# Kernel tuning notes

Hardware: AMD Instinct MI355X
Metric: run time of the kernel (lower is better)

Reference implementation:

```python
import jax, jax.numpy as jnp
import numpy as np

NPOINT, RADIUS, NSAMPLE = 512, 0.2, 32
MLP = [64, 64, 128]
IN_CH = 67
EPS = 1e-5


def farthest_point_sample(xyz, npoint):
    # xyz: [B, N, 3] -> idx [B, npoint]. Deterministic start at index 0.
    B, N, _ = xyz.shape

    def step(carry, _):
        dist, far = carry  # dist [B,N], far [B]
        centroid = jnp.take_along_axis(xyz, far[:, None, None], axis=1)  # [B,1,3]
        d = jnp.sum((xyz - centroid) ** 2, axis=-1)  # [B,N]
        dist = jnp.minimum(dist, d)
        return (dist, jnp.argmax(dist, axis=-1).astype(jnp.int32)), far

    init = (jnp.full((B, N), 1e10, dtype=xyz.dtype), jnp.zeros((B,), jnp.int32))
    _, idxs = jax.lax.scan(step, init, None, length=npoint)
    return idxs.T  # [B, npoint]


def query_ball_point(radius, nsample, xyz, new_xyz):
    # xyz [B,N,3], new_xyz [B,S,3] -> idx [B,S,nsample]
    B, N, _ = xyz.shape
    sqr = jnp.sum((new_xyz[:, :, None, :] - xyz[:, None, :, :]) ** 2, axis=-1)  # [B,S,N]
    gidx = jnp.where(sqr > radius * radius, N, jnp.arange(N, dtype=jnp.int32))
    gidx = jnp.sort(gidx, axis=-1)[:, :, :nsample]
    first = gidx[:, :, :1]
    return jnp.where(gidx == N, first, gidx).astype(jnp.int32)


def gather_points(pts, idx):
    # pts [B,N,C], idx [B,...] -> [B,...,C]
    return jax.vmap(lambda p, i: p[i])(pts, idx)


def sample_and_group(npoint, radius, nsample, xyz, points):
    fps_idx = farthest_point_sample(xyz, npoint)          # [B,S]
    new_xyz = gather_points(xyz, fps_idx)                 # [B,S,3]
    idx = query_ball_point(radius, nsample, xyz, new_xyz)  # [B,S,K]
    grouped_xyz = gather_points(xyz, idx)                 # [B,S,K,3]
    grouped_xyz_norm = grouped_xyz - new_xyz[:, :, None, :]
    grouped_pts = gather_points(points, idx)              # [B,S,K,D]
    new_points = jnp.concatenate([grouped_xyz_norm, grouped_pts], axis=-1)  # [B,S,K,3+D]
    return new_xyz, new_points


def mlp_bn_relu(x, w, b, gamma, beta):
    # x [B,C,K,S]; 1x1 conv + training-mode BatchNorm2d + ReLU
    y = jnp.einsum('oc,bcks->boks', w, x) + b[None, :, None, None]
    mean = jnp.mean(y, axis=(0, 2, 3), keepdims=True)
    var = jnp.var(y, axis=(0, 2, 3), keepdims=True)
    y = (y - mean) * jax.lax.rsqrt(var + EPS)
    y = y * gamma[None, :, None, None] + beta[None, :, None, None]
    return jax.nn.relu(y)


def setup_inputs() -> dict:
    key = jax.random.key(0)
    ks = jax.random.split(key, 8)
    B, N, D = 16, 2048, 64
    inp = {
        'xyz': jax.random.normal(ks[0], (B, 3, N), jnp.float32),
        'points': jax.random.normal(ks[1], (B, D, N), jnp.float32),
    }
    last = IN_CH
    for i, out in enumerate(MLP):
        kw = jax.random.fold_in(ks[2], i)
        inp[f'w{i}'] = jax.random.normal(kw, (out, last), jnp.float32) * 0.05
        inp[f'b{i}'] = jnp.zeros((out,), jnp.float32)
        inp[f'g{i}'] = jnp.ones((out,), jnp.float32)
        inp[f'bt{i}'] = jnp.zeros((out,), jnp.float32)
        last = out
    return inp


def reference(xyz, points, w0, b0, g0, bt0, w1, b1, g1, bt1, w2, b2, g2, bt2):
    # xyz [B,3,N], points [B,D,N]
    xyz_t = jnp.transpose(xyz, (0, 2, 1))      # [B,N,3]
    pts_t = jnp.transpose(points, (0, 2, 1))   # [B,N,D]
    new_xyz, new_points = sample_and_group(NPOINT, RADIUS, NSAMPLE, xyz_t, pts_t)
    # [B,S,K,C] -> [B,C,K,S]
    x = jnp.transpose(new_points, (0, 3, 2, 1))
    for (w, b, g, bt) in ((w0, b0, g0, bt0), (w1, b1, g1, bt1), (w2, b2, g2, bt2)):
        x = mlp_bn_relu(x, w, b, g, bt)
    feature = jnp.max(x, axis=2)               # [B,C',S]
    new_xyz_out = jnp.transpose(new_xyz, (0, 2, 1))  # [B,3,S]
    return new_xyz_out, feature
```

## Files before the change

kernel.cpp:

```cpp
#include <hip/hip_runtime.h>
#include <hip/hip_bf16.h>
#include <stdint.h>

#define NB 16
#define NPT 2048
#define NS 512
#define NK 32
#define PTOT (NB*NS*NK)
#define EPSV 1e-5f

typedef __attribute__((ext_vector_type(8))) short short8;
typedef __attribute__((ext_vector_type(4))) float floatx4;

#define WS_NEWXYZ 0
#define WS_ST     24576
#define WS_W1BF   30720
#define WS_W2BF   32768
#define WS_W0R    36864
#define WS_RAWMAX 39936
#define WS_PTS_TB 564224
#define WS_Y1     1612800
#define WS_Y2     10001408

__device__ __forceinline__ float bf2f(ushort u){ return __uint_as_float((uint32_t)u<<16); }
__device__ __forceinline__ ushort f2bf(float f){
  uint32_t u = __float_as_uint(f);
  return (ushort)((u + 0x7FFFu + ((u>>16)&1u)) >> 16);
}

template<int CTRL>
__device__ __forceinline__ double dppmax64f(double k){
  long long b = __double_as_longlong(k);
  int lo = (int)(uint32_t)b, hi = (int)(b>>32);
  int olo = __builtin_amdgcn_update_dpp(lo, lo, CTRL, 0xF, 0xF, false);
  int ohi = __builtin_amdgcn_update_dpp(hi, hi, CTRL, 0xF, 0xF, false);
  double o = __hiloint2double(ohi, olo);
  return fmax(o, k);
}
__device__ __forceinline__ unsigned long long u64max(unsigned long long a, unsigned long long b){ return a>b?a:b; }

template<int CTRL>
__device__ __forceinline__ float dppaddf(float v){
  int o = __builtin_amdgcn_update_dpp(__float_as_int(v), __float_as_int(v), CTRL, 0xF, 0xF, false);
  return v + __int_as_float(o);
}
__device__ __forceinline__ float rowsum16(float v){
  v = dppaddf<0xB1>(v);
  v = dppaddf<0x4E>(v);
  v = dppaddf<0x124>(v);
  v = dppaddf<0x128>(v);
  return v;
}

__global__ __launch_bounds__(256) void prep_kernel(const float* __restrict__ xyz,
    float* __restrict__ nxyz, float* __restrict__ out0,
    const float* __restrict__ pts, ushort* __restrict__ pts_tb,
    const float* __restrict__ w0, const float* __restrict__ w1, const float* __restrict__ w2,
    ushort* __restrict__ w0r, ushort* __restrict__ w1b, ushort* __restrict__ w2b,
    float* __restrict__ st)
{
  __shared__ union {
    struct { float4 lc[NPT]; double warr[2][4]; int sel[NS]; } f;
    float tile[64][65];
  } sm;
  const int blk = blockIdx.x;
  const int tid = threadIdx.x;
  if (blk < 16){
    const int b = blk;
    const float* xb = xyz + (size_t)b*3*NPT;
    float px[8], py[8], pz[8], dist[8];
    uint32_t lo_[8];
    #pragma unroll
    for (int j=0;j<8;j++){
      int n = j*256 + tid;
      float x = xb[n], y = xb[NPT+n], z = xb[2*NPT+n];
      sm.f.lc[n] = make_float4(x,y,z,0.f);
      px[j]=x; py[j]=y; pz[j]=z; dist[j]=1e10f;
      lo_[j] = ~(uint32_t)n;
    }
    if (tid==0) sm.f.sel[0]=0;
    __syncthreads();
    float4 c0 = sm.f.lc[0];
    float cx = c0.x, cy = c0.y, cz = c0.z;
    const int lane = tid & 63, wid = tid >> 6;
    for (int t=1;t<NS;t++){
      double kk[8];
      #pragma unroll
      for (int j=0;j<8;j++){
        float dx = __fsub_rn(px[j], cx);
        float dy = __fsub_rn(py[j], cy);
        float dz = __fsub_rn(pz[j], cz);
        float d  = __fadd_rn(__fadd_rn(__fmul_rn(dx,dx),__fmul_rn(dy,dy)),__fmul_rn(dz,dz));
        float dd = fminf(dist[j], d);
        dist[j] = dd;
        kk[j] = __hiloint2double((int)__float_as_uint(dd), (int)lo_[j]);
      }
      double m0 = fmax(kk[0],kk[1]), m1 = fmax(kk[2],kk[3]);
      double m2 = fmax(kk[4],kk[5]), m3 = fmax(kk[6],kk[7]);
      double best = fmax(fmax(m0,m1), fmax(m2,m3));
      best = dppmax64f<0xB1>(best);
      best = dppmax64f<0x4E>(best);
      best = dppmax64f<0x124>(best);
      best = dppmax64f<0x128>(best);
      long long bb = __double_as_longlong(best);
      int bl = (int)(uint32_t)bb, bh = (int)(bb>>32);
      unsigned long long k0 = (((unsigned long long)(uint32_t)__builtin_amdgcn_readlane(bh, 0))<<32)  | (uint32_t)__builtin_amdgcn_readlane(bl, 0);
      unsigned long long k1 = (((unsigned long long)(uint32_t)__builtin_amdgcn_readlane(bh, 16))<<32) | (uint32_t)__builtin_amdgcn_readlane(bl, 16);
      unsigned long long k2 = (((unsigned long long)(uint32_t)__builtin_amdgcn_readlane(bh, 32))<<32) | (uint32_t)__builtin_amdgcn_readlane(bl, 32);
      unsigned long long k3 = (((unsigned long long)(uint32_t)__builtin_amdgcn_readlane(bh, 48))<<32) | (uint32_t)__builtin_amdgcn_readlane(bl, 48);
      unsigned long long kw = u64max(u64max(k0,k1), u64max(k2,k3));
      if (lane==0) sm.f.warr[t&1][wid] = __longlong_as_double((long long)kw);
      __syncthreads();
      double w0_ = sm.f.warr[t&1][0], w1_ = sm.f.warr[t&1][1], w2_ = sm.f.warr[t&1][2], w3_ = sm.f.warr[t&1][3];
      double f = fmax(fmax(w0_,w1_), fmax(w2_,w3_));
      int n = (int)(~(uint32_t)__double_as_longlong(f));
      float4 cc = sm.f.lc[n];
      cx = cc.x; cy = cc.y; cz = cc.z;
      if (tid==0) sm.f.sel[t]=n;
    }
    __syncthreads();
    for (int s = tid; s < NS; s += 256){
      int n = sm.f.sel[s];
      float4 cc = sm.f.lc[n];
      float* np_ = nxyz + ((size_t)b*NS + s)*3;
      np_[0]=cc.x; np_[1]=cc.y; np_[2]=cc.z;
      float* ob = out0 + (size_t)b*3*NS + s;
      ob[0]=cc.x; ob[NS]=cc.y; ob[2*NS]=cc.z;
    }
  } else if (blk < 528){
    const int t2 = blk - 16;
    const int b = t2 >> 5;
    const int n0 = (t2 & 31) * 64;
    const int lane = tid & 63;
    const int row4 = tid >> 6;
    const float* src = pts + (size_t)b*64*NPT;
    #pragma unroll
    for (int r=0; r<16; r++){
      int cc = r*4 + row4;
      sm.tile[cc][lane] = src[(size_t)cc*NPT + n0 + lane];
    }
    __syncthreads();
    ushort* dst = pts_tb + ((size_t)b*NPT + n0)*64;
    #pragma unroll
    for (int r=0; r<16; r++){
      int nn = r*4 + row4;
      dst[(size_t)nn*64 + lane] = f2bf(sm.tile[lane][nn]);
    }
  } else {
    for (int i = tid; i < 4096; i += 256) w1b[i] = f2bf(w1[i]);
    for (int i = tid; i < 8192; i += 256) w2b[i] = f2bf(w2[i]);
    for (int i = tid; i < 6144; i += 256) st[i] = 0.f;
    for (int i = tid; i < 6144; i += 256){
      int o = i / 96, k = i - o*96;
      float v = (k < 64) ? w0[o*67 + 3 + k] : ((k < 67) ? w0[o*67 + (k-64)] : 0.f);
      w0r[i] = f2bf(v);
    }
  }
}

__global__ __launch_bounds__(256) void conv1_mfma(const float* __restrict__ xyz,
    const ushort* __restrict__ pts_tb, const float* __restrict__ nxyz,
    const ushort* __restrict__ w0r, const float* __restrict__ b0,
    ushort* __restrict__ y1, float* __restrict__ st)
{
  __shared__ int gq[4][NK];
  __shared__ float lsum[4][64], lsq[4][64];
  const int tid = threadIdx.x;
  const int wid = tid>>6, lane = tid&63;
  const int q = lane>>4, nn = lane&15;
  const int g = blockIdx.x*4 + wid;
  const int b = g >> 9;
  const float* xb = xyz + (size_t)b*3*NPT;
  const float* cgp = nxyz + (size_t)g*3;
  const float cx = cgp[0], cy = cgp[1], cz = cgp[2];
  {
    const float r2 = 0.2f*0.2f;
    uint32_t mymask = 0;
    #pragma unroll
    for (int ch=0; ch<NPT/64; ch++){
      int n = ch*64 + lane;
      float dx = __fsub_rn(cx, xb[n]);
      float dy = __fsub_rn(cy, xb[NPT+n]);
      float dz = __fsub_rn(cz, xb[2*NPT+n]);
      float d  = __fadd_rn(__fadd_rn(__fmul_rn(dx,dx),__fmul_rn(dy,dy)),__fmul_rn(dz,dz));
      if (d <= r2) mymask |= (1u<<ch);
    }
    int cnt = 0, first = 0;
    for (int ch=0; ch<NPT/64 && cnt<NK; ch++){
      bool in = (mymask>>ch) & 1u;
      unsigned long long mask = __ballot(in);
      if (mask){
        if (cnt==0) first = ch*64 + (__ffsll((unsigned long long)mask)-1);
        if (in){
          int pos = cnt + __popcll(mask & ((1ull<<lane)-1ull));
          if (pos < NK) gq[wid][pos] = ch*64 + lane;
        }
        cnt += __popcll(mask);
      }
    }
    if (cnt < NK && lane >= cnt && lane < NK) gq[wid][lane] = first;
  }
  int n0 = gq[wid][nn], n1 = gq[wid][16+nn];
  float dx0 = xb[n0]-cx, dy0 = xb[NPT+n0]-cy, dz0 = xb[2*NPT+n0]-cz;
  float dx1 = xb[n1]-cx, dy1 = xb[NPT+n1]-cy, dz1 = xb[2*NPT+n1]-cz;
  floatx4 z4 = {0.f,0.f,0.f,0.f};
  floatx4 acc[4][2];
  #pragma unroll
  for (int mt=0;mt<4;mt++){ acc[mt][0]=z4; acc[mt][1]=z4; }
  const ushort* pr0 = pts_tb + ((size_t)b*NPT + n0)*64;
  const ushort* pr1 = pts_tb + ((size_t)b*NPT + n1)*64;
  #pragma unroll
  for (int kh=0; kh<2; kh++){
    short8 B0 = *(const short8*)(pr0 + kh*32 + q*8);
    short8 B1 = *(const short8*)(pr1 + kh*32 + q*8);
    #pragma unroll
    for (int mt=0; mt<4; mt++){
      short8 A = *(const short8*)(w0r + (mt*16+nn)*96 + kh*32 + q*8);
      acc[mt][0] = __builtin_amdgcn_mfma_f32_16x16x32_bf16(A, B0, acc[mt][0], 0,0,0);
      acc[mt][1] = __builtin_amdgcn_mfma_f32_16x16x32_bf16(A, B1, acc[mt][1], 0,0,0);
    }
  }
  {
    short8 B0 = {0,0,0,0,0,0,0,0}, B1 = {0,0,0,0,0,0,0,0};
    if (q==0){
      B0[0]=(short)f2bf(dx0); B0[1]=(short)f2bf(dy0); B0[2]=(short)f2bf(dz0);
      B1[0]=(short)f2bf(dx1); B1[1]=(short)f2bf(dy1); B1[2]=(short)f2bf(dz1);
    }
    #pragma unroll
    for (int mt=0; mt<4; mt++){
      short8 A = *(const short8*)(w0r + (mt*16+nn)*96 + 64 + q*8);
      acc[mt][0] = __builtin_amdgcn_mfma_f32_16x16x32_bf16(A, B0, acc[mt][0], 0,0,0);
      acc[mt][1] = __builtin_amdgcn_mfma_f32_16x16x32_bf16(A, B1, acc[mt][1], 0,0,0);
    }
  }
  float ss[4][4], sq2[4][4];
  #pragma unroll
  for (int mt=0;mt<4;mt++)
    #pragma unroll
    for (int r=0;r<4;r++){ ss[mt][r]=0.f; sq2[mt][r]=0.f; }
  #pragma unroll
  for (int nt=0; nt<2; nt++){
    int p = g*32 + nt*16 + nn;
    #pragma unroll
    for (int mt=0; mt<4; mt++){
      float v0 = acc[mt][nt][0] + b0[mt*16 + q*4 + 0];
      float v1 = acc[mt][nt][1] + b0[mt*16 + q*4 + 1];
      float v2 = acc[mt][nt][2] + b0[mt*16 + q*4 + 2];
      float v3 = acc[mt][nt][3] + b0[mt*16 + q*4 + 3];
      ss[mt][0]+=v0; ss[mt][1]+=v1; ss[mt][2]+=v2; ss[mt][3]+=v3;
      sq2[mt][0]=fmaf(v0,v0,sq2[mt][0]); sq2[mt][1]=fmaf(v1,v1,sq2[mt][1]);
      sq2[mt][2]=fmaf(v2,v2,sq2[mt][2]); sq2[mt][3]=fmaf(v3,v3,sq2[mt][3]);
      uint2 wv;
      wv.x = (uint32_t)f2bf(v0) | ((uint32_t)f2bf(v1)<<16);
      wv.y = (uint32_t)f2bf(v2) | ((uint32_t)f2bf(v3)<<16);
      *(uint2*)(y1 + (size_t)p*64 + mt*16 + q*4) = wv;
    }
  }
  #pragma unroll
  for (int mt=0;mt<4;mt++)
    #pragma unroll
    for (int r=0;r<4;r++){
      float sv = rowsum16(ss[mt][r]);
      float qv = rowsum16(sq2[mt][r]);
      if (nn==0){ lsum[wid][mt*16+q*4+r] = sv; lsq[wid][mt*16+q*4+r] = qv; }
    }
  __syncthreads();
  if (tid < 64){
    float s = lsum[0][tid]+lsum[1][tid]+lsum[2][tid]+lsum[3][tid];
    float q2v = lsq[0][tid]+lsq[1][tid]+lsq[2][tid]+lsq[3][tid];
    int rep = blockIdx.x & 15;
    atomicAdd(&st[rep*128 + tid], s);
    atomicAdd(&st[rep*128 + 64 + tid], q2v);
  }
}

__global__ __launch_bounds__(256) void conv2_mfma(const ushort* __restrict__ yin,
    float* __restrict__ st, const float* __restrict__ g0, const float* __restrict__ bt0,
    const ushort* __restrict__ Wb, const float* __restrict__ bias,
    ushort* __restrict__ yout)
{
  __shared__ float aAl[64], aBl[64];
  __shared__ float lsum[4][64], lsq[4][64];
  const int tid = threadIdx.x;
  if (tid < 64){
    float s=0.f, qv=0.f;
    #pragma unroll
    for (int r=0;r<16;r++){ s += st[r*128 + tid]; qv += st[r*128 + 64 + tid]; }
    float mean = s * (1.f/PTOT);
    float var  = qv * (1.f/PTOT) - mean*mean;
    float a = g0[tid] * rsqrtf(var + EPSV);
    aAl[tid] = a;
    aBl[tid] = fmaf(-mean, a, bt0[tid]);
  }
  __syncthreads();
  const int wid = tid>>6, lane = tid&63;
  const int q = lane>>4, nn = lane&15;
  const int p0 = (blockIdx.x*4 + wid) * 32;
  float a_[2][8], b_[2][8];
  #pragma unroll
  for (int kh=0;kh<2;kh++)
    #pragma unroll
    for (int j=0;j<8;j++){
      a_[kh][j] = aAl[kh*32 + q*8 + j];
      b_[kh][j] = aBl[kh*32 + q*8 + j];
    }
  short8 Af[4][2];
  #pragma unroll
  for (int mt=0;mt<4;mt++)
    #pragma unroll
    for (int kh=0;kh<2;kh++)
      Af[mt][kh] = *(const short8*)(Wb + (mt*16 + nn)*64 + kh*32 + q*8);
  float bias_[4][4];
  #pragma unroll
  for (int mt=0;mt<4;mt++)
    #pragma unroll
    for (int r=0;r<4;r++) bias_[mt][r] = bias[mt*16 + q*4 + r];
  floatx4 z = {0.f,0.f,0.f,0.f};
  floatx4 acc[4][2];
  #pragma unroll
  for (int mt=0;mt<4;mt++){ acc[mt][0]=z; acc[mt][1]=z; }
  #pragma unroll
  for (int nt=0;nt<2;nt++){
    #pragma unroll
    for (int kh=0;kh<2;kh++){
      short8 raw = *(const short8*)(yin + (size_t)(p0 + nt*16 + nn)*64 + kh*32 + q*8);
      short8 bf;
      #pragma unroll
      for (int j=0;j<8;j++){
        float f = bf2f((ushort)raw[j]);
        f = fmaxf(fmaf(f, a_[kh][j], b_[kh][j]), 0.f);
        bf[j] = (short)f2bf(f);
      }
      #pragma unroll
      for (int mt=0;mt<4;mt++)
        acc[mt][nt] = __builtin_amdgcn_mfma_f32_16x16x32_bf16(Af[mt][kh], bf, acc[mt][nt], 0,0,0);
    }
  }
  float ss[4][4], sq2[4][4];
  #pragma unroll
  for (int mt=0;mt<4;mt++)
    #pragma unroll
    for (int r=0;r<4;r++){ ss[mt][r]=0.f; sq2[mt][r]=0.f; }
  #pragma unroll
  for (int nt=0;nt<2;nt++){
    int p = p0 + nt*16 + nn;
    #pragma unroll
    for (int mt=0;mt<4;mt++){
      float v0 = acc[mt][nt][0] + bias_[mt][0];
      float v1 = acc[mt][nt][1] + bias_[mt][1];
      float v2 = acc[mt][nt][2] + bias_[mt][2];
      float v3 = acc[mt][nt][3] + bias_[mt][3];
      ss[mt][0]+=v0; ss[mt][1]+=v1; ss[mt][2]+=v2; ss[mt][3]+=v3;
      sq2[mt][0]=fmaf(v0,v0,sq2[mt][0]); sq2[mt][1]=fmaf(v1,v1,sq2[mt][1]);
      sq2[mt][2]=fmaf(v2,v2,sq2[mt][2]); sq2[mt][3]=fmaf(v3,v3,sq2[mt][3]);
      uint2 w;
      w.x = (uint32_t)f2bf(v0) | ((uint32_t)f2bf(v1)<<16);
      w.y = (uint32_t)f2bf(v2) | ((uint32_t)f2bf(v3)<<16);
      *(uint2*)(yout + (size_t)p*64 + mt*16 + q*4) = w;
    }
  }
  #pragma unroll
  for (int mt=0;mt<4;mt++)
    #pragma unroll
    for (int r=0;r<4;r++){
      float sv = rowsum16(ss[mt][r]);
      float qv = rowsum16(sq2[mt][r]);
      if (nn==0){ lsum[wid][mt*16+q*4+r] = sv; lsq[wid][mt*16+q*4+r] = qv; }
    }
  __syncthreads();
  if (tid < 64){
    float s = lsum[0][tid]+lsum[1][tid]+lsum[2][tid]+lsum[3][tid];
    float q2v = lsq[0][tid]+lsq[1][tid]+lsq[2][tid]+lsq[3][tid];
    int rep = blockIdx.x & 15;
    atomicAdd(&st[2048 + rep*128 + tid], s);
    atomicAdd(&st[2048 + rep*128 + 64 + tid], q2v);
  }
}

__global__ __launch_bounds__(256) void conv3_mfma(const ushort* __restrict__ yin,
    float* __restrict__ st, const float* __restrict__ g1, const float* __restrict__ bt1,
    const ushort* __restrict__ Wb, const float* __restrict__ bias,
    ushort* __restrict__ rawmax)
{
  __shared__ ushort tile[64*132];
  __shared__ float aAl[64], aBl[64];
  const int tid = threadIdx.x;
  if (tid < 64){
    float s=0.f, qv=0.f;
    #pragma unroll
    for (int r=0;r<16;r++){ s += st[2048 + r*128 + tid]; qv += st[2048 + r*128 + 64 + tid]; }
    float mean = s * (1.f/PTOT);
    float var  = qv * (1.f/PTOT) - mean*mean;
    float a = g1[tid] * rsqrtf(var + EPSV);
    aAl[tid] = a;
    aBl[tid] = fmaf(-mean, a, bt1[tid]);
  }
  __syncthreads();
  const int wid = tid>>6, lane = tid&63;
  const int q = lane>>4, nn = lane&15;
  const int p0 = (blockIdx.x*4 + wid) * 16;
  float a_[2][8], b_[2][8];
  #pragma unroll
  for (int kh=0;kh<2;kh++)
    #pragma unroll
    for (int j=0;j<8;j++){
      a_[kh][j] = aAl[kh*32 + q*8 + j];
      b_[kh][j] = aBl[kh*32 + q*8 + j];
    }
  short8 bfr[2];
  #pragma unroll
  for (int kh=0;kh<2;kh++){
    short8 raw = *(const short8*)(yin + (size_t)(p0 + nn)*64 + kh*32 + q*8);
    short8 bf;
    #pragma unroll
    for (int j=0;j<8;j++){
      float f = bf2f((ushort)raw[j]);
      f = fmaxf(fmaf(f, a_[kh][j], b_[kh][j]), 0.f);
      bf[j] = (short)f2bf(f);
    }
    bfr[kh] = bf;
  }
  #pragma unroll 1
  for (int mh=0;mh<2;mh++){
    floatx4 z = {0.f,0.f,0.f,0.f};
    floatx4 acc[4];
    short8 Af[4][2];
    #pragma unroll
    for (int mt=0;mt<4;mt++){
      acc[mt]=z;
      #pragma unroll
      for (int kh=0;kh<2;kh++)
        Af[mt][kh] = *(const short8*)(Wb + ((mh*4+mt)*16 + nn)*64 + kh*32 + q*8);
    }
    #pragma unroll
    for (int kh=0;kh<2;kh++)
      #pragma unroll
      for (int mt=0;mt<4;mt++)
        acc[mt] = __builtin_amdgcn_mfma_f32_16x16x32_bf16(Af[mt][kh], bfr[kh], acc[mt], 0,0,0);
    #pragma unroll
    for (int mt=0;mt<4;mt++){
      int m0 = (mh*4+mt)*16;
      float v0 = acc[mt][0] + bias[m0 + q*4 + 0];
      float v1 = acc[mt][1] + bias[m0 + q*4 + 1];
      float v2 = acc[mt][2] + bias[m0 + q*4 + 2];
      float v3 = acc[mt][3] + bias[m0 + q*4 + 3];
      uint2 w;
      w.x = (uint32_t)f2bf(v0) | ((uint32_t)f2bf(v1)<<16);
      w.y = (uint32_t)f2bf(v2) | ((uint32_t)f2bf(v3)<<16);
      *(uint2*)&tile[(wid*16 + nn)*132 + m0 + q*4] = w;
    }
  }
  __syncthreads();
  const int c = tid >> 1, half = tid & 1;
  float s = 0.f, q2 = 0.f, mx = -1e30f;
  #pragma unroll 4
  for (int it=0; it<32; it++){
    float f = bf2f(tile[(half*32 + it)*132 + c]);
    s += f; q2 = fmaf(f,f,q2); mx = fmaxf(mx, f);
  }
  rawmax[(size_t)(blockIdx.x*2 + half)*128 + c] = f2bf(mx);
  s  += __shfl_xor(s, 1, 64);
  q2 += __shfl_xor(q2, 1, 64);
  if (half==0){
    int rep = blockIdx.x & 7;
    atomicAdd(&st[4096 + rep*128 + c], s);
    atomicAdd(&st[5120 + rep*128 + c], q2);
  }
}

__global__ __launch_bounds__(256) void finalize_kernel(const ushort* __restrict__ rawmax,
    const float* __restrict__ st, const float* __restrict__ g2, const float* __restrict__ bt2,
    float* __restrict__ out)
{
  __shared__ float tile[64][65];
  __shared__ float aAl[128], aBl[128];
  const int tid = threadIdx.x;
  if (tid < 128){
    float s=0.f, qv=0.f;
    #pragma unroll
    for (int r=0;r<8;r++){ s += st[4096 + r*128 + tid]; qv += st[5120 + r*128 + tid]; }
    float mean = s * (1.f/PTOT);
    float var  = qv * (1.f/PTOT) - mean*mean;
    float a = g2[tid] * rsqrtf(var + EPSV);
    aAl[tid] = a;
    aBl[tid] = fmaf(-mean, a, bt2[tid]);
  }
  __syncthreads();
  const int b  = blockIdx.x >> 4;
  const int ct = (blockIdx.x >> 3) & 1;
  const int stt = blockIdx.x & 7;
  const int c0 = ct*64, s0 = stt*64;
  const int lane = tid & 63, wid = tid >> 6;
  #pragma unroll
  for (int r=0;r<16;r++){
    int sl = r*4 + wid;
    tile[sl][lane] = bf2f(rawmax[((size_t)(b*512 + s0 + sl))*128 + c0 + lane]);
  }
  __syncthreads();
  #pragma unroll
  for (int r=0;r<16;r++){
    int cl = r*4 + wid;
    float a = aAl[c0+cl], bb = aBl[c0+cl];
    out[((size_t)(b*128 + c0 + cl))*512 + s0 + lane] = fmaxf(fmaf(tile[lane][cl], a, bb), 0.f);
  }
}

extern "C" void kernel_launch(void* const* d_in, const int* in_sizes, int n_in,
                              void* d_out, int out_size, void* d_ws, size_t ws_size,
                              hipStream_t stream) {
  const float* xyz = (const float*)d_in[0];
  const float* pts = (const float*)d_in[1];
  const float* w0  = (const float*)d_in[2];
  const float* b0  = (const float*)d_in[3];
  const float* g0  = (const float*)d_in[4];
  const float* bt0 = (const float*)d_in[5];
  const float* w1  = (const float*)d_in[6];
  const float* b1  = (const float*)d_in[7];
  const float* g1  = (const float*)d_in[8];
  const float* bt1 = (const float*)d_in[9];
  const float* w2  = (const float*)d_in[10];
  const float* b2  = (const float*)d_in[11];
  const float* g2  = (const float*)d_in[12];
  const float* bt2 = (const float*)d_in[13];
  float* out = (float*)d_out;
  float* ws  = (float*)d_ws;

  float* nxyz = ws + WS_NEWXYZ;
  float* st   = ws + WS_ST;
  ushort* w0r = (ushort*)(ws + WS_W0R);
  ushort* w1b = (ushort*)(ws + WS_W1BF);
  ushort* w2b = (ushort*)(ws + WS_W2BF);
  ushort* rawmax = (ushort*)(ws + WS_RAWMAX);
  ushort* pts_tb = (ushort*)(ws + WS_PTS_TB);
  ushort* y1 = (ushort*)(ws + WS_Y1);
  ushort* y2 = (ushort*)(ws + WS_Y2);

  prep_kernel<<<529,256,0,stream>>>(xyz, nxyz, out, pts, pts_tb, w0, w1, w2, w0r, w1b, w2b, st);
  conv1_mfma<<<2048,256,0,stream>>>(xyz, pts_tb, nxyz, w0r, b0, y1, st);
  conv2_mfma<<<2048,256,0,stream>>>(y1, st, g0, bt0, w1b, b1, y2);
  conv3_mfma<<<4096,256,0,stream>>>(y2, st, g1, bt1, w2b, b2, rawmax);
  finalize_kernel<<<256,256,0,stream>>>(rawmax, st, g2, bt2, out + NB*3*NS);
}
```

Measured before the change: 416.1 us.

## Run farthest point sampling in a single wavefront to remove block barriers

The FPS loop now runs on one 64-lane wavefront holding 32 points per lane, instead of four wavefronts with 8 points each that met at a __syncthreads every iteration. The cross-lane argmax uses row_bcast DPP steps plus a single readlane of lane 63, dropping the shared-memory exchange and the barrier from each of the 511 serial steps. In exchange each iteration does four times more work per lane and uses many more registers, and the other three wavefronts sit idle during FPS.

Result: slower. 513.3 us (+23.4%).

```diff
diff --git a/kernel.cpp b/kernel.cpp
--- a/kernel.cpp
+++ b/kernel.cpp
@@ -37,7 +37,6 @@
   double o = __hiloint2double(ohi, olo);
   return fmax(o, k);
 }
-__device__ __forceinline__ unsigned long long u64max(unsigned long long a, unsigned long long b){ return a>b?a:b; }
 
 template<int CTRL>
 __device__ __forceinline__ float dppaddf(float v){
@@ -60,63 +59,67 @@
     float* __restrict__ st)
 {
   __shared__ union {
-    struct { float4 lc[NPT]; double warr[2][4]; int sel[NS]; } f;
+    struct { float4 lc[NPT]; int sel[NS]; } f;
     float tile[64][65];
   } sm;
   const int blk = blockIdx.x;
   const int tid = threadIdx.x;
   if (blk < 16){
     const int b = blk;
+    const int lane = tid & 63, wid = tid >> 6;
     const float* xb = xyz + (size_t)b*3*NPT;
-    float px[8], py[8], pz[8], dist[8];
-    uint32_t lo_[8];
     #pragma unroll
     for (int j=0;j<8;j++){
       int n = j*256 + tid;
-      float x = xb[n], y = xb[NPT+n], z = xb[2*NPT+n];
-      sm.f.lc[n] = make_float4(x,y,z,0.f);
-      px[j]=x; py[j]=y; pz[j]=z; dist[j]=1e10f;
-      lo_[j] = ~(uint32_t)n;
+      sm.f.lc[n] = make_float4(xb[n], xb[NPT+n], xb[2*NPT+n], 0.f);
     }
     if (tid==0) sm.f.sel[0]=0;
     __syncthreads();
-    float4 c0 = sm.f.lc[0];
-    float cx = c0.x, cy = c0.y, cz = c0.z;
-    const int lane = tid & 63, wid = tid >> 6;
-    for (int t=1;t<NS;t++){
-      double kk[8];
+    if (wid==0){
+      float px[32], py[32], pz[32], dist[32];
+      uint32_t lo_[32];
       #pragma unroll
-      for (int j=0;j<8;j++){
-        float dx = __fsub_rn(px[j], cx);
-        float dy = __fsub_rn(py[j], cy);
-        float dz = __fsub_rn(pz[j], cz);
-        float d  = __fadd_rn(__fadd_rn(__fmul_rn(dx,dx),__fmul_rn(dy,dy)),__fmul_rn(dz,dz));
-        float dd = fminf(dist[j], d);
-        dist[j] = dd;
-        kk[j] = __hiloint2double((int)__float_as_uint(dd), (int)lo_[j]);
+      for (int j=0;j<32;j++){
+        int n = j*64 + lane;
+        px[j]=xb[n]; py[j]=xb[NPT+n]; pz[j]=xb[2*NPT+n];
+        dist[j]=1e10f;
+        lo_[j] = ~(uint32_t)n;
       }
-      double m0 = fmax(kk[0],kk[1]), m1 = fmax(kk[2],kk[3]);
-      double m2 = fmax(kk[4],kk[5]), m3 = fmax(kk[6],kk[7]);
-      double best = fmax(fmax(m0,m1), fmax(m2,m3));
-      best = dppmax64f<0xB1>(best);
-      best = dppmax64f<0x4E>(best);
-      best = dppmax64f<0x124>(best);
-      best = dppmax64f<0x128>(best);
-      long long bb = __double_as_longlong(best);
-      int bl = (int)(uint32_t)bb, bh = (int)(bb>>32);
-      unsigned long long k0 = (((unsigned long long)(uint32_t)__builtin_amdgcn_readlane(bh, 0))<<32)  | (uint32_t)__builtin_amdgcn_readlane(bl, 0);
-      unsigned long long k1 = (((unsigned long long)(uint32_t)__builtin_amdgcn_readlane(bh, 16))<<32) | (uint32_t)__builtin_amdgcn_readlane(bl, 16);
-      unsigned long long k2 = (((unsigned long long)(uint32_t)__builtin_amdgcn_readlane(bh, 32))<<32) | (uint32_t)__builtin_amdgcn_readlane(bl, 32);
-      unsigned long long k3 = (((unsigned long long)(uint32_t)__builtin_amdgcn_readlane(bh, 48))<<32) | (uint32_t)__builtin_amdgcn_readlane(bl, 48);
-      unsigned long long kw = u64max(u64max(k0,k1), u64max(k2,k3));
-      if (lane==0) sm.f.warr[t&1][wid] = __longlong_as_double((long long)kw);
-      __syncthreads();
-      double w0_ = sm.f.warr[t&1][0], w1_ = sm.f.warr[t&1][1], w2_ = sm.f.warr[t&1][2], w3_ = sm.f.warr[t&1][3];
-      double f = fmax(fmax(w0_,w1_), fmax(w2_,w3_));
-      int n = (int)(~(uint32_t)__double_as_longlong(f));
-      float4 cc = sm.f.lc[n];
-      cx = cc.x; cy = cc.y; cz = cc.z;
-      if (tid==0) sm.f.sel[t]=n;
+      float4 c0 = sm.f.lc[0];
+      float cx = c0.x, cy = c0.y, cz = c0.z;
+      for (int t=1;t<NS;t++){
+        double b0a = -1.0, b1a = -1.0, b2a = -1.0, b3a = -1.0;
+        #pragma unroll
+        for (int j=0;j<32;j+=4){
+          #pragma unroll
+          for (int u=0;u<4;u++){
+            float dx = __fsub_rn(px[j+u], cx);
+            float dy = __fsub_rn(py[j+u], cy);
+            float dz = __fsub_rn(pz[j+u], cz);
+            float d  = __fadd_rn(__fadd_rn(__fmul_rn(dx,dx),__fmul_rn(dy,dy)),__fmul_rn(dz,dz));
+            float dd = fminf(dist[j+u], d);
+            dist[j+u] = dd;
+            double k = __hiloint2double((int)__float_as_uint(dd), (int)lo_[j+u]);
+            if (u==0) b0a = fmax(b0a, k);
+            else if (u==1) b1a = fmax(b1a, k);
+            else if (u==2) b2a = fmax(b2a, k);
+            else b3a = fmax(b3a, k);
+          }
+        }
+        double best = fmax(fmax(b0a,b1a), fmax(b2a,b3a));
+        best = dppmax64f<0xB1>(best);
+        best = dppmax64f<0x4E>(best);
+        best = dppmax64f<0x124>(best);
+        best = dppmax64f<0x128>(best);
+        best = dppmax64f<0x142>(best);
+        best = dppmax64f<0x143>(best);
+        long long bb = __double_as_longlong(best);
+        uint32_t lo63 = (uint32_t)__builtin_amdgcn_readlane((int)(uint32_t)bb, 63);
+        int n = (int)(~lo63);
+        float4 cc = sm.f.lc[n];
+        cx = cc.x; cy = cc.y; cz = cc.z;
+        if (lane==0) sm.f.sel[t]=n;
+      }
     }
     __syncthreads();
     for (int s = tid; s < NS; s += 256){
```
